# Kernel tuning notes

Measured on AMD Instinct MI355X. Metric: run time of the kernel, lower is better.

Reference implementation:

```python
import jax, jax.numpy as jnp
import numpy as np

N, E, H, C, HC = 16384, 262144, 4, 128, 512
G, IN, ED, OUT, NCLS = 8, 5, 2, 256, 12
EPS = 1e-5


def _gatv2(x, src, dst, ea, Wl, Wr, We, att, b):
    # GATv2Conv (PyG): score = att . leaky_relu(lin_l(x_j) + lin_r(x_i) + lin_e(e))
    xl = (x @ Wl).reshape(-1, H, C)          # source transform [N,H,C]
    xr = (x @ Wr).reshape(-1, H, C)          # target transform [N,H,C]
    ee = (ea @ We).reshape(-1, H, C)         # edge embedding   [E,H,C]
    s = jax.nn.leaky_relu(xl[src] + xr[dst] + ee, 0.2)
    logit = jnp.einsum('ehc,hc->eh', s, att)            # [E,H]
    m = jax.ops.segment_max(logit, dst, num_segments=N)  # per-dst max
    a = jnp.exp(logit - m[dst])
    denom = jax.ops.segment_sum(a, dst, num_segments=N)
    alpha = a / (denom[dst] + 1e-16)                     # segment softmax
    out = jax.ops.segment_sum(xl[src] * alpha[:, :, None], dst, num_segments=N)
    return out.reshape(-1, HC) + b


def _bn(x, g, b):  # BatchNorm1d, training-mode batch stats
    mu = x.mean(0)
    var = x.var(0)
    return g * (x - mu) * jax.lax.rsqrt(var + EPS) + b


def setup_inputs() -> dict:
    key = jax.random.key(0)
    ks = iter(jax.random.split(key, 32))
    d = {}
    d['x'] = jax.random.normal(next(ks), (N, IN), jnp.float32)
    d['edge_attr'] = jax.random.normal(next(ks), (E, ED), jnp.float32)
    d['edge_index'] = jax.random.randint(next(ks), (2, E), 0, N)
    d['batch'] = jnp.sort(jax.random.randint(next(ks), (N,), 0, G))
    for i, din in zip((1, 2, 3), (IN, HC, HC)):
        d[f'c{i}_Wl'] = jax.random.normal(next(ks), (din, HC), jnp.float32) * 0.05
        d[f'c{i}_Wr'] = jax.random.normal(next(ks), (din, HC), jnp.float32) * 0.05
        d[f'c{i}_We'] = jax.random.normal(next(ks), (ED, HC), jnp.float32) * 0.05
        d[f'c{i}_att'] = jax.random.normal(next(ks), (H, C), jnp.float32) * 0.05
        d[f'c{i}_b'] = jnp.zeros((HC,), jnp.float32)
        d[f'bn{i}_g'] = jnp.ones((HC,), jnp.float32)
        d[f'bn{i}_b'] = jnp.zeros((HC,), jnp.float32)
    d['ge_W1'] = jax.random.normal(next(ks), (HC, OUT), jnp.float32) * 0.05
    d['ge_b1'] = jnp.zeros((OUT,), jnp.float32)
    d['ge_W2'] = jax.random.normal(next(ks), (OUT, OUT), jnp.float32) * 0.05
    d['ge_b2'] = jnp.zeros((OUT,), jnp.float32)
    d['cls_W'] = jax.random.normal(next(ks), (OUT, NCLS), jnp.float32) * 0.05
    d['cls_b'] = jnp.zeros((NCLS,), jnp.float32)
    return d


def reference(x, edge_attr, edge_index, batch,
              c1_Wl, c1_Wr, c1_We, c1_att, c1_b, bn1_g, bn1_b,
              c2_Wl, c2_Wr, c2_We, c2_att, c2_b, bn2_g, bn2_b,
              c3_Wl, c3_Wr, c3_We, c3_att, c3_b, bn3_g, bn3_b,
              ge_W1, ge_b1, ge_W2, ge_b2, cls_W, cls_b):
    src, dst = edge_index[0], edge_index[1]
    x1 = jax.nn.elu(_bn(_gatv2(x, src, dst, edge_attr, c1_Wl, c1_Wr, c1_We, c1_att, c1_b), bn1_g, bn1_b))
    x2 = jax.nn.elu(_bn(_gatv2(x1, src, dst, edge_attr, c2_Wl, c2_Wr, c2_We, c2_att, c2_b), bn2_g, bn2_b)) + x1
    x3 = jax.nn.elu(_bn(_gatv2(x2, src, dst, edge_attr, c3_Wl, c3_Wr, c3_We, c3_att, c3_b), bn3_g, bn3_b)) + x2
    cnt = jax.ops.segment_sum(jnp.ones((N,), x3.dtype), batch, num_segments=G)
    x_pool = jax.ops.segment_sum(x3, batch, num_segments=G) / cnt[:, None]
    emb = jax.nn.relu(x_pool @ ge_W1 + ge_b1) @ ge_W2 + ge_b2
    logits = emb @ cls_W + cls_b
    return logits, emb
```

## Files before the change

### kernel.cpp

```cpp
#include <hip/hip_runtime.h>
#include <math.h>

#define NN    16384
#define NE    262144
#define NHEAD 4
#define HC    512
#define NG    8

typedef __bf16 bf16x8 __attribute__((ext_vector_type(8)));
typedef float floatx4 __attribute__((ext_vector_type(4)));
typedef float f32x2 __attribute__((ext_vector_type(2)));

__device__ __forceinline__ f32x2 sp2(float s) { return (f32x2){s, s}; }
__device__ __forceinline__ f32x2 pkmax(f32x2 a, f32x2 b) {
    f32x2 r; r.x = fmaxf(a.x, b.x); r.y = fmaxf(a.y, b.y); return r;
}

__device__ __forceinline__ unsigned short f2bf(float f) {
    union { float f; unsigned u; } v{f};
    unsigned r = v.u + 0x7FFFu + ((v.u >> 16) & 1u);
    return (unsigned short)(r >> 16);
}
__device__ __forceinline__ float bf2f(unsigned short b) {
    return __uint_as_float((unsigned)b << 16);
}

__device__ __forceinline__ void unpk8v(uint4 v, f32x2* f) {
    f[0] = (f32x2){__uint_as_float(v.x << 16), __uint_as_float(v.x & 0xFFFF0000u)};
    f[1] = (f32x2){__uint_as_float(v.y << 16), __uint_as_float(v.y & 0xFFFF0000u)};
    f[2] = (f32x2){__uint_as_float(v.z << 16), __uint_as_float(v.z & 0xFFFF0000u)};
    f[3] = (f32x2){__uint_as_float(v.w << 16), __uint_as_float(v.w & 0xFFFF0000u)};
}

__global__ void k_hist(const int* __restrict__ dst, int* __restrict__ cnt) {
    int e = blockIdx.x * 256 + threadIdx.x;
    if (e < NE) atomicAdd(&cnt[dst[e]], 1);
}

__global__ __launch_bounds__(1024) void k_scan(const int* __restrict__ cnt,
                                               int* __restrict__ rp,
                                               int* __restrict__ offp,
                                               const int* __restrict__ batch,
                                               int* __restrict__ gcnt) {
    __shared__ int part[1024];
    int t = threadIdx.x;
    if (t < NG) {
        int lb[2];
#pragma unroll
        for (int q = 0; q < 2; q++) {
            int target = t + q;
            int lo = 0, hi = NN;
            while (lo < hi) {
                int mid = (lo + hi) >> 1;
                if (batch[mid] < target) lo = mid + 1; else hi = mid;
            }
            lb[q] = lo;
        }
        gcnt[t] = lb[1] - lb[0];
    }
    int base = t * 16;
    int loc[16];
    int s = 0;
#pragma unroll
    for (int i = 0; i < 16; i++) { loc[i] = s; s += cnt[base + i]; }
    part[t] = s;
    __syncthreads();
    for (int off = 1; off < 1024; off <<= 1) {
        int v = 0;
        if (t >= off) v = part[t - off];
        __syncthreads();
        if (t >= off) part[t] += v;
        __syncthreads();
    }
    int excl = (t == 0) ? 0 : part[t - 1];
#pragma unroll
    for (int i = 0; i < 16; i++) {
        int r = excl + loc[i];
        rp[base + i] = r;
        offp[base + i] = r;
    }
    if (t == 1023) rp[NN] = excl + s;
}

__global__ void k_fill(const int* __restrict__ dst, const int* __restrict__ src,
                       const float* __restrict__ ea, int* __restrict__ offp,
                       int* __restrict__ csrc, float2* __restrict__ ce) {
    int e = blockIdx.x * 256 + threadIdx.x;
    if (e < NE) {
        int d = dst[e];
        int pos = atomicAdd(&offp[d], 1);
        csrc[pos] = src[e];
        ce[pos] = *(const float2*)(ea + 2 * (size_t)e);
    }
}

__global__ __launch_bounds__(256) void k_lin1(const float* __restrict__ x,
                                              const float* __restrict__ Wl,
                                              const float* __restrict__ Wr,
                                              unsigned short* __restrict__ xl,
                                              unsigned short* __restrict__ xr) {
    int n = blockIdx.x * 4 + (threadIdx.x >> 6);
    int lane = threadIdx.x & 63;
    int j0 = lane << 3;
    float xs[5];
#pragma unroll
    for (int k = 0; k < 5; k++) xs[k] = x[n * 5 + k];
    float al[8] = {}, ar[8] = {};
#pragma unroll
    for (int k = 0; k < 5; k++) {
        float4 wl0 = *(const float4*)(Wl + k * 512 + j0);
        float4 wl1 = *(const float4*)(Wl + k * 512 + j0 + 4);
        float4 wr0 = *(const float4*)(Wr + k * 512 + j0);
        float4 wr1 = *(const float4*)(Wr + k * 512 + j0 + 4);
        al[0] += xs[k] * wl0.x; al[1] += xs[k] * wl0.y; al[2] += xs[k] * wl0.z; al[3] += xs[k] * wl0.w;
        al[4] += xs[k] * wl1.x; al[5] += xs[k] * wl1.y; al[6] += xs[k] * wl1.z; al[7] += xs[k] * wl1.w;
        ar[0] += xs[k] * wr0.x; ar[1] += xs[k] * wr0.y; ar[2] += xs[k] * wr0.z; ar[3] += xs[k] * wr0.w;
        ar[4] += xs[k] * wr1.x; ar[5] += xs[k] * wr1.y; ar[6] += xs[k] * wr1.z; ar[7] += xs[k] * wr1.w;
    }
    ushort4 o0, o1;
    o0.x = f2bf(al[0]); o0.y = f2bf(al[1]); o0.z = f2bf(al[2]); o0.w = f2bf(al[3]);
    o1.x = f2bf(al[4]); o1.y = f2bf(al[5]); o1.z = f2bf(al[6]); o1.w = f2bf(al[7]);
    *(ushort4*)(xl + (size_t)n * 512 + j0) = o0;
    *(ushort4*)(xl + (size_t)n * 512 + j0 + 4) = o1;
    o0.x = f2bf(ar[0]); o0.y = f2bf(ar[1]); o0.z = f2bf(ar[2]); o0.w = f2bf(ar[3]);
    o1.x = f2bf(ar[4]); o1.y = f2bf(ar[5]); o1.z = f2bf(ar[6]); o1.w = f2bf(ar[7]);
    *(ushort4*)(xr + (size_t)n * 512 + j0) = o0;
    *(ushort4*)(xr + (size_t)n * 512 + j0 + 4) = o1;
}

__global__ __launch_bounds__(256) void k_wt4(const float* __restrict__ W0,
                                             const float* __restrict__ W1,
                                             const float* __restrict__ W2,
                                             const float* __restrict__ W3,
                                             unsigned short* __restrict__ Wt2,
                                             unsigned short* __restrict__ Wt3) {
    __shared__ float tile[64][65];
    int bid = blockIdx.x;
    int mat = bid >> 6, sub = bid & 63;
    const float* W = (mat == 0) ? W0 : (mat == 1) ? W1 : (mat == 2) ? W2 : W3;
    unsigned short* Wt = (mat == 0) ? Wt2 : (mat == 1) ? (Wt2 + 512 * 512)
                       : (mat == 2) ? Wt3 : (Wt3 + 512 * 512);
    int n0 = (sub & 7) * 64, k0 = (sub >> 3) * 64;
    int lr = threadIdx.x >> 4;
    int lc = (threadIdx.x & 15) << 2;
    for (int r = lr; r < 64; r += 16) {
        float4 v = *(const float4*)(W + (size_t)(k0 + r) * 512 + n0 + lc);
        tile[r][lc] = v.x; tile[r][lc + 1] = v.y; tile[r][lc + 2] = v.z; tile[r][lc + 3] = v.w;
    }
    __syncthreads();
    for (int r = lr; r < 64; r += 16) {
        ushort4 o;
        o.x = f2bf(tile[lc + 0][r]); o.y = f2bf(tile[lc + 1][r]);
        o.z = f2bf(tile[lc + 2][r]); o.w = f2bf(tile[lc + 3][r]);
        *(ushort4*)(Wt + (size_t)(n0 + r) * 512 + k0 + lc) = o;
    }
}

#define BM 128
#define BN 128
#define BK 64
#define LDK 72

__global__ __launch_bounds__(256) void k_gemm_bf16(
        const unsigned short* __restrict__ Ab,
        const unsigned short* __restrict__ Bt,
        unsigned short* __restrict__ xl, unsigned short* __restrict__ xr) {
    __shared__ unsigned short As[BM * LDK];
    __shared__ unsigned short Bs[BN * LDK];
    int t = threadIdx.x;
    int bid = blockIdx.x;
    int xcd = bid & 7, r = bid >> 3;
    int m0 = (xcd * 16 + (r & 15)) * BM;
    int n0 = (r >> 4) * BN;
    int wid = t >> 6, lane = t & 63;
    int wm = (wid >> 1) * 64, wn = (wid & 1) * 64;
    int lrow = lane & 15, quad = lane >> 4;
    floatx4 acc[4][4] = {};
    for (int k0 = 0; k0 < 512; k0 += BK) {
        __syncthreads();
#pragma unroll
        for (int it = 0; it < 4; it++) {
            int cid = it * 256 + t;
            int row = cid >> 3, ch = cid & 7;
            uint4 va = *(const uint4*)(Ab + (size_t)(m0 + row) * 512 + k0 + ch * 8);
            *(uint4*)&As[row * LDK + ch * 8] = va;
            uint4 vb = *(const uint4*)(Bt + (size_t)(n0 + row) * 512 + k0 + ch * 8);
            *(uint4*)&Bs[row * LDK + ch * 8] = vb;
        }
        __syncthreads();
#pragma unroll
        for (int ko = 0; ko < 2; ko++) {
            bf16x8 af[4], bfr[4];
#pragma unroll
            for (int i = 0; i < 4; i++) {
                af[i]  = *(const bf16x8*)&As[(wm + i * 16 + lrow) * LDK + ko * 32 + quad * 8];
                bfr[i] = *(const bf16x8*)&Bs[(wn + i * 16 + lrow) * LDK + ko * 32 + quad * 8];
            }
#pragma unroll
            for (int i = 0; i < 4; i++)
#pragma unroll
                for (int j = 0; j < 4; j++)
                    acc[i][j] = __builtin_amdgcn_mfma_f32_16x16x32_bf16(af[i], bfr[j], acc[i][j], 0, 0, 0);
        }
    }
#pragma unroll
    for (int i = 0; i < 4; i++) {
        int row = m0 + wm + i * 16 + quad * 4;
#pragma unroll
        for (int j = 0; j < 4; j++) {
            int col = n0 + wn + j * 16 + lrow;
            unsigned short* dstp = (col < 512) ? (xl + (size_t)row * 512 + col)
                                               : (xr + (size_t)row * 512 + (col - 512));
#pragma unroll
            for (int rr = 0; rr < 4; rr++) dstp[(size_t)rr * 512] = f2bf(acc[i][j][rr]);
        }
    }
}

__global__ __launch_bounds__(256) void k_attn(
        const unsigned short* __restrict__ xl, const unsigned short* __restrict__ xr,
        const int* __restrict__ rp, const int* __restrict__ csrc,
        const float2* __restrict__ ce, const float* __restrict__ We,
        const float* __restrict__ att, const float* __restrict__ bias,
        unsigned short* __restrict__ out) {
    int n = blockIdx.x * 4 + (threadIdx.x >> 6);
    int lane = threadIdx.x & 63;
    int c0 = lane << 3;
    f32x2 wv0[4], wv1[4], av[4], rv[4];
    {
        float4 a = *(const float4*)(We + c0), b = *(const float4*)(We + c0 + 4);
        wv0[0] = (f32x2){a.x, a.y}; wv0[1] = (f32x2){a.z, a.w};
        wv0[2] = (f32x2){b.x, b.y}; wv0[3] = (f32x2){b.z, b.w};
        a = *(const float4*)(We + 512 + c0); b = *(const float4*)(We + 512 + c0 + 4);
        wv1[0] = (f32x2){a.x, a.y}; wv1[1] = (f32x2){a.z, a.w};
        wv1[2] = (f32x2){b.x, b.y}; wv1[3] = (f32x2){b.z, b.w};
        a = *(const float4*)(att + c0); b = *(const float4*)(att + c0 + 4);
        av[0] = (f32x2){a.x, a.y}; av[1] = (f32x2){a.z, a.w};
        av[2] = (f32x2){b.x, b.y}; av[3] = (f32x2){b.z, b.w};
        uint4 vr = *(const uint4*)(xr + (size_t)n * 512 + c0);
        unpk8v(vr, rv);
    }
    float l = 0.f;
    f32x2 acc[4] = {sp2(0.f), sp2(0.f), sp2(0.f), sp2(0.f)};
    int beg = rp[n], end = rp[n + 1];
    uint4 cv0 = {}, cv1 = {};
    float2 ce0 = {}, ce1 = {};
    if (beg < end) {
        int i1 = (beg + 1 < end) ? beg + 1 : end - 1;
        cv0 = *(const uint4*)(xl + (size_t)csrc[beg] * 512 + c0);
        ce0 = ce[beg];
        cv1 = *(const uint4*)(xl + (size_t)csrc[i1] * 512 + c0);
        ce1 = ce[i1];
    }
    int i = beg;
    for (; i + 1 < end; i += 2) {
        uint4 a0 = cv0, a1 = cv1;
        float2 d0 = ce0, d1 = ce1;
        int q0 = i + 2, q1 = i + 3;
        q0 = (q0 < end) ? q0 : end - 1;
        q1 = (q1 < end) ? q1 : end - 1;
        cv0 = *(const uint4*)(xl + (size_t)csrc[q0] * 512 + c0);
        ce0 = ce[q0];
        cv1 = *(const uint4*)(xl + (size_t)csrc[q1] * 512 + c0);
        ce1 = ce[q1];
        f32x2 lv0[4], lv1[4];
        unpk8v(a0, lv0);
        unpk8v(a1, lv1);
        f32x2 d0x = sp2(d0.x), d0y = sp2(d0.y), d1x = sp2(d1.x), d1y = sp2(d1.y);
        f32x2 p0v = sp2(0.f), p1v = sp2(0.f);
#pragma unroll
        for (int j = 0; j < 4; j++) {
            f32x2 v0 = lv0[j] + rv[j] + d0x * wv0[j] + d0y * wv1[j];
            f32x2 v1 = lv1[j] + rv[j] + d1x * wv0[j] + d1y * wv1[j];
            v0 = pkmax(v0, sp2(0.2f) * v0);
            v1 = pkmax(v1, sp2(0.2f) * v1);
            p0v += av[j] * v0;
            p1v += av[j] * v1;
        }
        float p0 = p0v.x + p0v.y;
        float p1 = p1v.x + p1v.y;
        p0 += __shfl_xor(p0, 1);  p1 += __shfl_xor(p1, 1);
        p0 += __shfl_xor(p0, 2);  p1 += __shfl_xor(p1, 2);
        p0 += __shfl_xor(p0, 4);  p1 += __shfl_xor(p1, 4);
        p0 += __shfl_xor(p0, 8);  p1 += __shfl_xor(p1, 8);
        float w0 = __expf(fminf(p0, 60.f));
        float w1 = __expf(fminf(p1, 60.f));
        l += w0 + w1;
        f32x2 w0v = sp2(w0), w1v = sp2(w1);
#pragma unroll
        for (int j = 0; j < 4; j++)
            acc[j] += w0v * lv0[j] + w1v * lv1[j];
    }
    if (i < end) {
        f32x2 lv[4];
        unpk8v(cv0, lv);
        f32x2 dx = sp2(ce0.x), dy = sp2(ce0.y);
        f32x2 pv = sp2(0.f);
#pragma unroll
        for (int j = 0; j < 4; j++) {
            f32x2 v = lv[j] + rv[j] + dx * wv0[j] + dy * wv1[j];
            v = pkmax(v, sp2(0.2f) * v);
            pv += av[j] * v;
        }
        float p = pv.x + pv.y;
        p += __shfl_xor(p, 1);
        p += __shfl_xor(p, 2);
        p += __shfl_xor(p, 4);
        p += __shfl_xor(p, 8);
        float w = __expf(fminf(p, 60.f));
        l += w;
        f32x2 wv = sp2(w);
#pragma unroll
        for (int j = 0; j < 4; j++) acc[j] += wv * lv[j];
    }
    float inv = 1.f / (l + 1e-16f);
    const float* bb = bias + c0;
    float4 b0 = *(const float4*)bb, b1 = *(const float4*)(bb + 4);
    ushort4 o0, o1;
    o0.x = f2bf(acc[0].x * inv + b0.x); o0.y = f2bf(acc[0].y * inv + b0.y);
    o0.z = f2bf(acc[1].x * inv + b0.z); o0.w = f2bf(acc[1].y * inv + b0.w);
    o1.x = f2bf(acc[2].x * inv + b1.x); o1.y = f2bf(acc[2].y * inv + b1.y);
    o1.z = f2bf(acc[3].x * inv + b1.z); o1.w = f2bf(acc[3].y * inv + b1.w);
    *(ushort4*)(out + (size_t)n * 512 + c0) = o0;
    *(ushort4*)(out + (size_t)n * 512 + c0 + 4) = o1;
}

__global__ __launch_bounds__(256) void k_bnstat(const unsigned short* __restrict__ xb,
                                                double* __restrict__ sum,
                                                double* __restrict__ sumsq) {
    int t = threadIdx.x;
    int r0 = blockIdx.x * 64;
    int c2 = t << 1;
    float s0 = 0.f, s1 = 0.f, q0 = 0.f, q1 = 0.f;
    for (int r = r0; r < r0 + 64; r++) {
        unsigned u = *(const unsigned*)(xb + (size_t)r * 512 + c2);
        float v0 = __uint_as_float(u << 16);
        float v1 = __uint_as_float(u & 0xFFFF0000u);
        s0 += v0; q0 += v0 * v0;
        s1 += v1; q1 += v1 * v1;
    }
    atomicAdd(sum + c2, (double)s0);
    atomicAdd(sum + c2 + 1, (double)s1);
    atomicAdd(sumsq + c2, (double)q0);
    atomicAdd(sumsq + c2 + 1, (double)q1);
}

__global__ void k_bnapply(const unsigned short* __restrict__ v,
                          const unsigned short* __restrict__ resid,
                          const double* __restrict__ sum, const double* __restrict__ sumsq,
                          const float* __restrict__ g, const float* __restrict__ beta,
                          unsigned short* __restrict__ outb) {
    int i = (blockIdx.x * 256 + threadIdx.x) << 2;
    int c = i & 511;
    ushort4 vu = *(const ushort4*)(v + i);
    double2 s01 = *(const double2*)(sum + c);
    double2 s23 = *(const double2*)(sum + c + 2);
    double2 q01 = *(const double2*)(sumsq + c);
    double2 q23 = *(const double2*)(sumsq + c + 2);
    float4 gg = *(const float4*)(g + c);
    float4 be = *(const float4*)(beta + c);
    const double invN = 1.0 / NN;
    double mu0 = s01.x * invN, mu1 = s01.y * invN, mu2 = s23.x * invN, mu3 = s23.y * invN;
    float sc0 = gg.x * rsqrtf((float)(q01.x * invN - mu0 * mu0) + 1e-5f);
    float sc1 = gg.y * rsqrtf((float)(q01.y * invN - mu1 * mu1) + 1e-5f);
    float sc2 = gg.z * rsqrtf((float)(q23.x * invN - mu2 * mu2) + 1e-5f);
    float sc3 = gg.w * rsqrtf((float)(q23.y * invN - mu3 * mu3) + 1e-5f);
    float y0 = (bf2f(vu.x) - (float)mu0) * sc0 + be.x;
    float y1 = (bf2f(vu.y) - (float)mu1) * sc1 + be.y;
    float y2 = (bf2f(vu.z) - (float)mu2) * sc2 + be.z;
    float y3 = (bf2f(vu.w) - (float)mu3) * sc3 + be.w;
    y0 = y0 > 0.f ? y0 : expm1f(y0);
    y1 = y1 > 0.f ? y1 : expm1f(y1);
    y2 = y2 > 0.f ? y2 : expm1f(y2);
    y3 = y3 > 0.f ? y3 : expm1f(y3);
    if (resid) {
        ushort4 ru = *(const ushort4*)(resid + i);
        y0 += bf2f(ru.x); y1 += bf2f(ru.y); y2 += bf2f(ru.z); y3 += bf2f(ru.w);
    }
    ushort4 o;
    o.x = f2bf(y0); o.y = f2bf(y1); o.z = f2bf(y2); o.w = f2bf(y3);
    *(ushort4*)(outb + i) = o;
}

__global__ __launch_bounds__(256) void k_pool(const unsigned short* __restrict__ xb,
                                              const int* __restrict__ batch,
                                              float* __restrict__ pooled) {
    __shared__ float lacc[NG][512];
    int t = threadIdx.x;
    for (int i = t; i < NG * 512; i += 256) ((float*)lacc)[i] = 0.f;
    __syncthreads();
    int r0 = blockIdx.x * 64;
    int c2 = t << 1;
    for (int r = r0; r < r0 + 64; r++) {
        int g = batch[r];
        unsigned u = *(const unsigned*)(xb + (size_t)r * 512 + c2);
        lacc[g][c2]     += __uint_as_float(u << 16);
        lacc[g][c2 + 1] += __uint_as_float(u & 0xFFFF0000u);
    }
    __syncthreads();
    int gmin = batch[r0], gmax = batch[r0 + 63];
    for (int g = gmin; g <= gmax; g++)
        for (int i = t; i < 512; i += 256)
            atomicAdd(&pooled[g * 512 + i], lacc[g][i]);
}

__global__ __launch_bounds__(256) void k_head_h1(const float* __restrict__ pooled,
                                                 const float* __restrict__ W1,
                                                 float* __restrict__ h1acc) {
    int g = blockIdx.x >> 4, s = blockIdx.x & 15;
    int o = threadIdx.x;
    int c0 = s * 32;
    float acc = 0.f;
#pragma unroll
    for (int c = 0; c < 32; c++)
        acc += pooled[g * 512 + c0 + c] * W1[(size_t)(c0 + c) * 256 + o];
    atomicAdd(&h1acc[g * 256 + o], acc);
}

__global__ __launch_bounds__(256) void k_head_emb(const float* __restrict__ h1acc,
                                                  const int* __restrict__ gcnt,
                                                  const float* __restrict__ b1,
                                                  const float* __restrict__ W2,
                                                  float* __restrict__ embacc) {
    __shared__ float hs[32];
    int g = blockIdx.x >> 3, s = blockIdx.x & 7;
    int c0 = s * 32;
    int t = threadIdx.x;
    if (t < 32) {
        float inv = 1.f / (float)gcnt[g];
        hs[t] = fmaxf(h1acc[g * 256 + c0 + t] * inv + b1[c0 + t], 0.f);
    }
    __syncthreads();
    float acc = 0.f;
#pragma unroll
    for (int c = 0; c < 32; c++)
        acc += hs[c] * W2[(size_t)(c0 + c) * 256 + t];
    atomicAdd(&embacc[g * 256 + t], acc);
}

__global__ __launch_bounds__(256) void k_head_fin(const float* __restrict__ embacc,
                                                  const float* __restrict__ b2,
                                                  const float* __restrict__ clsW,
                                                  const float* __restrict__ clsb,
                                                  float* __restrict__ outp) {
    __shared__ float es[256];
    int g = blockIdx.x, o = threadIdx.x;
    float e = embacc[g * 256 + o] + b2[o];
    outp[NG * 12 + g * 256 + o] = e;
    es[o] = e;
    __syncthreads();
    if (o < 12) {
        float lg = clsb[o];
        for (int c = 0; c < 256; c++) lg += es[c] * clsW[c * 12 + o];
        outp[g * 12 + o] = lg;
    }
}

extern "C" void kernel_launch(void* const* d_in, const int* in_sizes, int n_in,
                              void* d_out, int out_size, void* d_ws, size_t ws_size,
                              hipStream_t stream) {
    const float* x     = (const float*)d_in[0];
    const float* ea    = (const float*)d_in[1];
    const int*   ei    = (const int*)d_in[2];
    const int*   batch = (const int*)d_in[3];
    const int* src = ei;
    const int* dst = ei + NE;

    float* base = (float*)d_ws;
    size_t off = 0;
    auto alloc = [&](size_t n) -> float* {
        float* p = base + off;
        off += (n + 255) & ~(size_t)255;
        return p;
    };
    unsigned short* xl  = (unsigned short*)alloc((size_t)NN * 256);
    unsigned short* xr  = (unsigned short*)alloc((size_t)NN * 256);
    unsigned short* Yb  = (unsigned short*)alloc((size_t)NN * 256);
    unsigned short* XbA = (unsigned short*)alloc((size_t)NN * 256);
    unsigned short* XbB = (unsigned short*)alloc((size_t)NN * 256);
    unsigned short* Wt2 = (unsigned short*)alloc(512 * 1024 / 2);
    unsigned short* Wt3 = (unsigned short*)alloc(512 * 1024 / 2);
    int*      rp    = (int*)alloc(NN + 1);
    int*      offp  = (int*)alloc(NN);
    int*      csrc  = (int*)alloc(NE);
    float2*   ce    = (float2*)alloc((size_t)NE * 2);
    int*      cnt   = (int*)alloc(NN);
    double*   bsum3 = (double*)alloc(3 * 2048);
    float*    pooled= alloc(NG * 512);
    float*    h1acc = alloc(NG * 256);
    float*    embacc= alloc(NG * 256);
    int*      gcnt  = (int*)alloc(NG);
    float*    outp  = (float*)d_out;

    hipMemsetAsync(cnt, 0, 30720 * sizeof(float), stream);
    k_hist<<<NE / 256, 256, 0, stream>>>(dst, cnt);
    k_scan<<<1, 1024, 0, stream>>>(cnt, rp, offp, batch, gcnt);
    k_fill<<<NE / 256, 256, 0, stream>>>(dst, src, ea, offp, csrc, ce);
    k_wt4<<<256, 256, 0, stream>>>((const float*)d_in[11], (const float*)d_in[12],
                                   (const float*)d_in[18], (const float*)d_in[19], Wt2, Wt3);

    unsigned short* X = XbA;
    unsigned short* Xp = XbB;
    for (int l = 0; l < 3; l++) {
        const float* Wl  = (const float*)d_in[4 + l * 7 + 0];
        const float* Wr  = (const float*)d_in[4 + l * 7 + 1];
        const float* We  = (const float*)d_in[4 + l * 7 + 2];
        const float* att = (const float*)d_in[4 + l * 7 + 3];
        const float* cb  = (const float*)d_in[4 + l * 7 + 4];
        const float* bg  = (const float*)d_in[4 + l * 7 + 5];
        const float* bb  = (const float*)d_in[4 + l * 7 + 6];

        if (l == 0) {
            k_lin1<<<NN / 4, 256, 0, stream>>>(x, Wl, Wr, xl, xr);
        } else {
            k_gemm_bf16<<<1024, 256, 0, stream>>>(Xp, (l == 1) ? Wt2 : Wt3, xl, xr);
        }
        k_attn<<<NN / 4, 256, 0, stream>>>(xl, xr, rp, csrc, ce, We, att, cb, Yb);

        double* bsum = bsum3 + l * 1024;
        double* bsq  = bsum + 512;
        k_bnstat<<<256, 256, 0, stream>>>(Yb, bsum, bsq);
        k_bnapply<<<(size_t)NN * 512 / 1024, 256, 0, stream>>>(
            Yb, (l == 0) ? nullptr : Xp, bsum, bsq, bg, bb, X);

        unsigned short* tmp = Xp; Xp = X; X = tmp;
    }

    k_pool<<<NN / 64, 256, 0, stream>>>(Xp, batch, pooled);

    const float* geW1 = (const float*)d_in[25];
    const float* geb1 = (const float*)d_in[26];
    const float* geW2 = (const float*)d_in[27];
    const float* geb2 = (const float*)d_in[28];
    const float* clsW = (const float*)d_in[29];
    const float* clsb = (const float*)d_in[30];

    k_head_h1<<<NG * 16, 256, 0, stream>>>(pooled, geW1, h1acc);
    k_head_emb<<<NG * 8, 256, 0, stream>>>(h1acc, gcnt, geb1, geW2, embacc);
    k_head_fin<<<NG, 256, 0, stream>>>(embacc, geb2, clsW, clsb, outp);
}
```

Before: 479.6 us.

## Use direct global-to-LDS loads in GEMM and deepen attention gather prefetch

The GEMM tile loads now use global_load_lds to write straight into LDS without passing through registers, and the padded LDK stride is dropped so the layout matches the lane-contiguous write pattern. The attention kernel unrolls the edge loop to four edges per iteration with a four-deep prefetch of gathered xl rows, and marks the node index wave-uniform through readfirstlane. The deeper prefetch aims to hide gather latency but raises register pressure. The unpadded LDS layout may bring back bank conflicts on the MFMA fragment reads.

Measured after the change: 471.2 us. About the same (-1.7%).

```diff
diff --git a/kernel.cpp b/kernel.cpp
--- a/kernel.cpp
+++ b/kernel.cpp
@@ -31,6 +31,10 @@
     f[2] = (f32x2){__uint_as_float(v.z << 16), __uint_as_float(v.z & 0xFFFF0000u)};
     f[3] = (f32x2){__uint_as_float(v.w << 16), __uint_as_float(v.w & 0xFFFF0000u)};
 }
+
+#define GLD16(g, l) __builtin_amdgcn_global_load_lds( \
+    (const __attribute__((address_space(1))) void*)(g), \
+    (__attribute__((address_space(3))) void*)(l), 16, 0, 0)
 
 __global__ void k_hist(const int* __restrict__ dst, int* __restrict__ cnt) {
     int e = blockIdx.x * 256 + threadIdx.x;
@@ -159,14 +163,13 @@
 #define BM 128
 #define BN 128
 #define BK 64
-#define LDK 72
 
 __global__ __launch_bounds__(256) void k_gemm_bf16(
         const unsigned short* __restrict__ Ab,
         const unsigned short* __restrict__ Bt,
         unsigned short* __restrict__ xl, unsigned short* __restrict__ xr) {
-    __shared__ unsigned short As[BM * LDK];
-    __shared__ unsigned short Bs[BN * LDK];
+    __shared__ unsigned short As[BM * BK];
+    __shared__ unsigned short Bs[BN * BK];
     int t = threadIdx.x;
     int bid = blockIdx.x;
     int xcd = bid & 7, r = bid >> 3;
@@ -182,10 +185,8 @@
         for (int it = 0; it < 4; it++) {
             int cid = it * 256 + t;
             int row = cid >> 3, ch = cid & 7;
-            uint4 va = *(const uint4*)(Ab + (size_t)(m0 + row) * 512 + k0 + ch * 8);
-            *(uint4*)&As[row * LDK + ch * 8] = va;
-            uint4 vb = *(const uint4*)(Bt + (size_t)(n0 + row) * 512 + k0 + ch * 8);
-            *(uint4*)&Bs[row * LDK + ch * 8] = vb;
+            GLD16(Ab + (size_t)(m0 + row) * 512 + k0 + ch * 8, As + cid * 8);
+            GLD16(Bt + (size_t)(n0 + row) * 512 + k0 + ch * 8, Bs + cid * 8);
         }
         __syncthreads();
 #pragma unroll
@@ -193,8 +194,8 @@
             bf16x8 af[4], bfr[4];
 #pragma unroll
             for (int i = 0; i < 4; i++) {
-                af[i]  = *(const bf16x8*)&As[(wm + i * 16 + lrow) * LDK + ko * 32 + quad * 8];
-                bfr[i] = *(const bf16x8*)&Bs[(wn + i * 16 + lrow) * LDK + ko * 32 + quad * 8];
+                af[i]  = *(const bf16x8*)&As[(wm + i * 16 + lrow) * BK + ko * 32 + quad * 8];
+                bfr[i] = *(const bf16x8*)&Bs[(wn + i * 16 + lrow) * BK + ko * 32 + quad * 8];
             }
 #pragma unroll
             for (int i = 0; i < 4; i++)
@@ -223,7 +224,7 @@
         const float2* __restrict__ ce, const float* __restrict__ We,
         const float* __restrict__ att, const float* __restrict__ bias,
         unsigned short* __restrict__ out) {
-    int n = blockIdx.x * 4 + (threadIdx.x >> 6);
+    int n = __builtin_amdgcn_readfirstlane(blockIdx.x * 4 + (threadIdx.x >> 6));
     int lane = threadIdx.x & 63;
     int c0 = lane << 3;
     f32x2 wv0[4], wv1[4], av[4], rv[4];
@@ -243,75 +244,83 @@
     float l = 0.f;
     f32x2 acc[4] = {sp2(0.f), sp2(0.f), sp2(0.f), sp2(0.f)};
     int beg = rp[n], end = rp[n + 1];
-    uint4 cv0 = {}, cv1 = {};
-    float2 ce0 = {}, ce1 = {};
+    uint4 cv[4];
+    float2 cev[4];
     if (beg < end) {
-        int i1 = (beg + 1 < end) ? beg + 1 : end - 1;
-        cv0 = *(const uint4*)(xl + (size_t)csrc[beg] * 512 + c0);
-        ce0 = ce[beg];
-        cv1 = *(const uint4*)(xl + (size_t)csrc[i1] * 512 + c0);
-        ce1 = ce[i1];
+#pragma unroll
+        for (int k = 0; k < 4; k++) {
+            int q = beg + k; q = (q < end) ? q : end - 1;
+            cv[k] = *(const uint4*)(xl + (size_t)csrc[q] * 512 + c0);
+            cev[k] = ce[q];
+        }
     }
     int i = beg;
-    for (; i + 1 < end; i += 2) {
-        uint4 a0 = cv0, a1 = cv1;
-        float2 d0 = ce0, d1 = ce1;
-        int q0 = i + 2, q1 = i + 3;
-        q0 = (q0 < end) ? q0 : end - 1;
-        q1 = (q1 < end) ? q1 : end - 1;
-        cv0 = *(const uint4*)(xl + (size_t)csrc[q0] * 512 + c0);
-        ce0 = ce[q0];
-        cv1 = *(const uint4*)(xl + (size_t)csrc[q1] * 512 + c0);
-        ce1 = ce[q1];
-        f32x2 lv0[4], lv1[4];
-        unpk8v(a0, lv0);
-        unpk8v(a1, lv1);
-        f32x2 d0x = sp2(d0.x), d0y = sp2(d0.y), d1x = sp2(d1.x), d1y = sp2(d1.y);
-        f32x2 p0v = sp2(0.f), p1v = sp2(0.f);
+    for (; i + 3 < end; i += 4) {
+        uint4 a[4]; float2 d[4];
+#pragma unroll
+        for (int k = 0; k < 4; k++) { a[k] = cv[k]; d[k] = cev[k]; }
+#pragma unroll
+        for (int k = 0; k < 4; k++) {
+            int q = i + 4 + k; q = (q < end) ? q : end - 1;
+            cv[k] = *(const uint4*)(xl + (size_t)csrc[q] * 512 + c0);
+            cev[k] = ce[q];
+        }
+        f32x2 lv[4][4];
+#pragma unroll
+        for (int k = 0; k < 4; k++) unpk8v(a[k], lv[k]);
+        float p[4];
+#pragma unroll
+        for (int k = 0; k < 4; k++) {
+            f32x2 dx = sp2(d[k].x), dy = sp2(d[k].y);
+            f32x2 pv = sp2(0.f);
+#pragma unroll
+            for (int j = 0; j < 4; j++) {
+                f32x2 v = lv[k][j] + rv[j] + dx * wv0[j] + dy * wv1[j];
+                v = pkmax(v, sp2(0.2f) * v);
+                pv += av[j] * v;
+            }
+            p[k] = pv.x + pv.y;
+        }
+#pragma unroll
+        for (int m = 1; m <= 8; m <<= 1) {
+#pragma unroll
+            for (int k = 0; k < 4; k++) p[k] += __shfl_xor(p[k], m);
+        }
+        float w[4];
+#pragma unroll
+        for (int k = 0; k < 4; k++) { w[k] = __expf(fminf(p[k], 60.f)); l += w[k]; }
 #pragma unroll
         for (int j = 0; j < 4; j++) {
-            f32x2 v0 = lv0[j] + rv[j] + d0x * wv0[j] + d0y * wv1[j];
-            f32x2 v1 = lv1[j] + rv[j] + d1x * wv0[j] + d1y * wv1[j];
-            v0 = pkmax(v0, sp2(0.2f) * v0);
-            v1 = pkmax(v1, sp2(0.2f) * v1);
-            p0v += av[j] * v0;
-            p1v += av[j] * v1;
-        }
-        float p0 = p0v.x + p0v.y;
-        float p1 = p1v.x + p1v.y;
-        p0 += __shfl_xor(p0, 1);  p1 += __shfl_xor(p1, 1);
-        p0 += __shfl_xor(p0, 2);  p1 += __shfl_xor(p1, 2);
-        p0 += __shfl_xor(p0, 4);  p1 += __shfl_xor(p1, 4);
-        p0 += __shfl_xor(p0, 8);  p1 += __shfl_xor(p1, 8);
-        float w0 = __expf(fminf(p0, 60.f));
-        float w1 = __expf(fminf(p1, 60.f));
-        l += w0 + w1;
-        f32x2 w0v = sp2(w0), w1v = sp2(w1);
-#pragma unroll
-        for (int j = 0; j < 4; j++)
-            acc[j] += w0v * lv0[j] + w1v * lv1[j];
-    }
-    if (i < end) {
-        f32x2 lv[4];
-        unpk8v(cv0, lv);
-        f32x2 dx = sp2(ce0.x), dy = sp2(ce0.y);
-        f32x2 pv = sp2(0.f);
-#pragma unroll
-        for (int j = 0; j < 4; j++) {
-            f32x2 v = lv[j] + rv[j] + dx * wv0[j] + dy * wv1[j];
-            v = pkmax(v, sp2(0.2f) * v);
-            pv += av[j] * v;
-        }
-        float p = pv.x + pv.y;
-        p += __shfl_xor(p, 1);
-        p += __shfl_xor(p, 2);
-        p += __shfl_xor(p, 4);
-        p += __shfl_xor(p, 8);
-        float w = __expf(fminf(p, 60.f));
-        l += w;
-        f32x2 wv = sp2(w);
-#pragma unroll
-        for (int j = 0; j < 4; j++) acc[j] += wv * lv[j];
+            f32x2 t0 = sp2(w[0]) * lv[0][j] + sp2(w[1]) * lv[1][j];
+            f32x2 t1 = sp2(w[2]) * lv[2][j] + sp2(w[3]) * lv[3][j];
+            acc[j] += t0 + t1;
+        }
+    }
+    int rem = end - i;
+#pragma unroll
+    for (int k = 0; k < 3; k++) {
+        if (k < rem) {
+            f32x2 lv[4];
+            unpk8v(cv[k], lv);
+            f32x2 dx = sp2(cev[k].x), dy = sp2(cev[k].y);
+            f32x2 pv = sp2(0.f);
+#pragma unroll
+            for (int j = 0; j < 4; j++) {
+                f32x2 v = lv[j] + rv[j] + dx * wv0[j] + dy * wv1[j];
+                v = pkmax(v, sp2(0.2f) * v);
+                pv += av[j] * v;
+            }
+            float p = pv.x + pv.y;
+            p += __shfl_xor(p, 1);
+            p += __shfl_xor(p, 2);
+            p += __shfl_xor(p, 4);
+            p += __shfl_xor(p, 8);
+            float w = __expf(fminf(p, 60.f));
+            l += w;
+            f32x2 wv = sp2(w);
+#pragma unroll
+            for (int j = 0; j < 4; j++) acc[j] += wv * lv[j];
+        }
     }
     float inv = 1.f / (l + 1e-16f);
     const float* bb = bias + c0;
```
